# Performance work log

Measured on AMD Instinct MI355X. Metric: run time of the kernel, lower is better.

Reference implementation:

```python
import jax, jax.numpy as jnp
import numpy as np

DIM = 384
WIN = 7
HEADS = 12
HEAD_DIM = DIM // HEADS
N = WIN * WIN


def _relative_position_index(w):
    coords = np.stack(np.meshgrid(np.arange(w), np.arange(w), indexing='ij'))  # [2,w,w]
    cf = coords.reshape(2, -1)                                                 # [2,N]
    rel = cf[:, :, None] - cf[:, None, :]                                      # [2,N,N]
    rel = rel.transpose(1, 2, 0).copy()
    rel[:, :, 0] += w - 1
    rel[:, :, 1] += w - 1
    rel[:, :, 0] *= 2 * w - 1
    return jnp.asarray(rel.sum(-1), dtype=jnp.int32)                           # [N,N]


def setup_inputs() -> dict:
    key = jax.random.key(0)
    ks = jax.random.split(key, 6)
    B_ = 2048
    x = jax.random.normal(ks[0], (B_, N, DIM), dtype=jnp.float32)
    mask = jnp.zeros((64, N, N), dtype=bool)  # nW=64, all-unmasked but exercises mask path
    qkv_w = jax.random.normal(ks[1], (3 * DIM, DIM), dtype=jnp.float32) * 0.02
    qkv_b = jnp.zeros((3 * DIM,), dtype=jnp.float32)
    proj_w = jax.random.normal(ks[2], (DIM, DIM), dtype=jnp.float32) * 0.02
    proj_b = jnp.zeros((DIM,), dtype=jnp.float32)
    rpb_table = jax.random.normal(ks[3], ((2 * WIN - 1) ** 2, HEADS), dtype=jnp.float32) * 0.02
    rel_index = _relative_position_index(WIN)
    return {"x": x, "mask": mask, "qkv_w": qkv_w, "qkv_b": qkv_b,
            "proj_w": proj_w, "proj_b": proj_b, "rpb_table": rpb_table,
            "rel_index": rel_index}


def reference(x, mask, qkv_w, qkv_b, proj_w, proj_b, rpb_table, rel_index):
    B_, n, C = x.shape
    scale = HEAD_DIM ** -0.5
    # qkv projection -> [3, B, H, N, hd]
    qkv = (x @ qkv_w.T + qkv_b).reshape(B_, n, 3, HEADS, HEAD_DIM)
    qkv = jnp.transpose(qkv, (2, 0, 3, 1, 4))
    q, k, v = qkv[0], qkv[1], qkv[2]
    attn = jnp.einsum('bhnd,bhmd->bhnm', q, k) * scale  # [B,H,N,N]
    # relative position bias: gather [N*N,H] -> [H,N,N]
    bias = rpb_table[rel_index.reshape(-1)].reshape(n, n, HEADS)
    attn = attn + jnp.transpose(bias, (2, 0, 1))[None]
    nW = mask.shape[0]
    attn = attn.reshape(B_ // nW, nW, HEADS, n, n)
    attn = jnp.where(mask[None, :, None], -jnp.inf, attn)
    attn = attn.reshape(B_, HEADS, n, n)
    attn = jax.nn.softmax(attn, axis=-1)
    out = jnp.einsum('bhnm,bhmd->bnhd', attn, v).reshape(B_, n, C)
    return out @ proj_w.T + proj_b
```

## Files before the change

kernel.cpp:

```cpp
#include <hip/hip_runtime.h>
#include <stdint.h>

#define HEADS 12
#define HD 32
#define NTOK 49
#define DIM 384
#define SCALE 0.17677669529663687f

typedef __attribute__((ext_vector_type(8))) short s8v;
typedef __attribute__((ext_vector_type(4))) float f4v;

__device__ __forceinline__ unsigned short f2bf(float f) {
    union { float f; unsigned int i; } c; c.f = f;
    unsigned int x = c.i;
    return (unsigned short)((x + 0x7FFFu + ((x >> 16) & 1u)) >> 16);
}

__device__ __forceinline__ s8v load_pack8(const float* p) {
    float4 a = *(const float4*)p;
    float4 b = *(const float4*)(p + 4);
    s8v r;
    r[0] = (short)f2bf(a.x); r[1] = (short)f2bf(a.y);
    r[2] = (short)f2bf(a.z); r[3] = (short)f2bf(a.w);
    r[4] = (short)f2bf(b.x); r[5] = (short)f2bf(b.y);
    r[6] = (short)f2bf(b.z); r[7] = (short)f2bf(b.w);
    return r;
}

#define QFRAGS (12 * 12 * 6 * 64)
#define PFRAGS (12 * 24 * 64)
__device__ s8v qpack_g[QFRAGS];
__device__ s8v ppack_g[PFRAGS];

__global__ __launch_bounds__(256) void prepack(
    const float* __restrict__ qkvw, const float* __restrict__ projw)
{
    int t = blockIdx.x * 256 + threadIdx.x;
    if (t < QFRAGS) {
        int lane = t & 63, fid = t >> 6;
        int nt = fid % 6, ks = (fid / 6) % 12, h = fid / 72;
        int l15 = lane & 15, lq = lane >> 4;
        int c96 = nt * 16 + l15;
        int sect = c96 >> 5, cc = c96 & 31;
        const float* src = qkvw + (size_t)(sect * DIM + h * HD + cc) * DIM + ks * 32 + lq * 8;
        float s = (sect == 0) ? SCALE : 1.0f;
        float4 a = *(const float4*)src;
        float4 b = *(const float4*)(src + 4);
        s8v r;
        r[0] = (short)f2bf(a.x * s); r[1] = (short)f2bf(a.y * s);
        r[2] = (short)f2bf(a.z * s); r[3] = (short)f2bf(a.w * s);
        r[4] = (short)f2bf(b.x * s); r[5] = (short)f2bf(b.y * s);
        r[6] = (short)f2bf(b.z * s); r[7] = (short)f2bf(b.w * s);
        qpack_g[t] = r;
    } else if (t < QFRAGS + PFRAGS) {
        int u = t - QFRAGS;
        int lane = u & 63, fid = u >> 6;
        int ct = fid % 24, h = fid / 24;
        int l15 = lane & 15, lq = lane >> 4;
        const float* src = projw + (size_t)(ct * 16 + l15) * DIM + h * HD + lq * 8;
        ppack_g[u] = load_pack8(src);
    }
}

#define QK_OFF 0
#define VT_OFF 5120
#define PL_OFF 7424
#define HO_OFF 12032
#define LDS_TOT 14592

__global__ __launch_bounds__(256, 2) void winattn_fused(
    const float* __restrict__ xg,
    const unsigned char* __restrict__ maskg,
    const float* __restrict__ qkvb,
    const float* __restrict__ projb,
    const float* __restrict__ rpb,
    const int*   __restrict__ relidx,
    float*       __restrict__ outg)
{
    __shared__ __align__(16) unsigned short lds[LDS_TOT];
    const int tid = threadIdx.x;
    const int w   = tid >> 6;
    const int l   = tid & 63;
    const int l15 = l & 15;
    const int lq  = l >> 4;
    const int b   = blockIdx.x;

    const float*         xw    = xg + (size_t)b * (NTOK * DIM);
    const unsigned char* maskw = maskg + (size_t)(b & 63) * (NTOK * NTOK);

    const int arow = min(w * 16 + l15, NTOK - 1);
    s8v xa[12];
#pragma unroll
    for (int ks = 0; ks < 12; ++ks)
        xa[ks] = load_pack8(xw + arow * DIM + ks * 32 + lq * 8);

    int boff[4][4];
#pragma unroll
    for (int nt = 0; nt < 4; ++nt)
#pragma unroll
        for (int reg = 0; reg < 4; ++reg) {
            int i = w * 16 + lq * 4 + reg;
            int j = nt * 16 + l15;
            if (i < NTOK && j < NTOK)
                boff[nt][reg] = maskw[i * NTOK + j] ? -1 : relidx[i * NTOK + j] * (HEADS * 4);
            else
                boff[nt][reg] = (j >= NTOK) ? -1 : 0;
        }

    const f4v fz = {0.f, 0.f, 0.f, 0.f};
    f4v oc[4][6];
#pragma unroll
    for (int mt = 0; mt < 4; ++mt)
#pragma unroll
        for (int j = 0; j < 6; ++j) oc[mt][j] = fz;

    for (int h = 0; h < HEADS; ++h) {
        const s8v* qp = qpack_g + (size_t)h * (12 * 6 * 64) + l;
        f4v acc[6];
#pragma unroll
        for (int nt = 0; nt < 6; ++nt) acc[nt] = fz;
#pragma unroll
        for (int ks = 0; ks < 12; ++ks) {
            s8v a = xa[ks];
            s8v b0 = qp[(ks * 6 + 0) * 64];
            s8v b1 = qp[(ks * 6 + 1) * 64];
            s8v b2 = qp[(ks * 6 + 2) * 64];
            s8v b3 = qp[(ks * 6 + 3) * 64];
            s8v b4 = qp[(ks * 6 + 4) * 64];
            s8v b5 = qp[(ks * 6 + 5) * 64];
            acc[0] = __builtin_amdgcn_mfma_f32_16x16x32_bf16(a, b0, acc[0], 0, 0, 0);
            acc[1] = __builtin_amdgcn_mfma_f32_16x16x32_bf16(a, b1, acc[1], 0, 0, 0);
            acc[2] = __builtin_amdgcn_mfma_f32_16x16x32_bf16(a, b2, acc[2], 0, 0, 0);
            acc[3] = __builtin_amdgcn_mfma_f32_16x16x32_bf16(a, b3, acc[3], 0, 0, 0);
            acc[4] = __builtin_amdgcn_mfma_f32_16x16x32_bf16(a, b4, acc[4], 0, 0, 0);
            acc[5] = __builtin_amdgcn_mfma_f32_16x16x32_bf16(a, b5, acc[5], 0, 0, 0);
        }

        __syncthreads();

#pragma unroll
        for (int nt = 0; nt < 6; ++nt) {
            int c96 = nt * 16 + l15;
            int sect = c96 >> 5;
            int cc = c96 & 31;
            float bias = qkvb[sect * DIM + h * HD + cc];
            if (sect == 0) bias *= SCALE;
#pragma unroll
            for (int reg = 0; reg < 4; ++reg) {
                int row = w * 16 + lq * 4 + reg;
                float v = acc[nt][reg] + bias;
                unsigned short bv = f2bf(v);
                if (sect < 2) lds[QK_OFF + sect * 2560 + row * 40 + cc] = bv;
                else          lds[VT_OFF + cc * 72 + row] = bv;
            }
        }
        __syncthreads();

        s8v qa = *(const s8v*)(&lds[QK_OFF + (w * 16 + l15) * 40 + lq * 8]);
        f4v sc[4];
#pragma unroll
        for (int nt = 0; nt < 4; ++nt) {
            s8v kb = *(const s8v*)(&lds[QK_OFF + 2560 + (nt * 16 + l15) * 40 + lq * 8]);
            sc[nt] = __builtin_amdgcn_mfma_f32_16x16x32_bf16(qa, kb, fz, 0, 0, 0);
        }
        const char* rpbb = (const char*)rpb + h * 4;
#pragma unroll
        for (int nt = 0; nt < 4; ++nt)
#pragma unroll
            for (int reg = 0; reg < 4; ++reg) {
                int bo = boff[nt][reg];
                float v = sc[nt][reg] + *(const float*)(rpbb + (bo < 0 ? 0 : bo));
                sc[nt][reg] = (bo < 0) ? -1e30f : v;
            }
#pragma unroll
        for (int reg = 0; reg < 4; ++reg) {
            float m = fmaxf(fmaxf(sc[0][reg], sc[1][reg]), fmaxf(sc[2][reg], sc[3][reg]));
            m = fmaxf(m, __shfl_xor(m, 1));
            m = fmaxf(m, __shfl_xor(m, 2));
            m = fmaxf(m, __shfl_xor(m, 4));
            m = fmaxf(m, __shfl_xor(m, 8));
            float e0 = __expf(sc[0][reg] - m);
            float e1 = __expf(sc[1][reg] - m);
            float e2 = __expf(sc[2][reg] - m);
            float e3 = __expf(sc[3][reg] - m);
            float t = (e0 + e1) + (e2 + e3);
            t += __shfl_xor(t, 1);
            t += __shfl_xor(t, 2);
            t += __shfl_xor(t, 4);
            t += __shfl_xor(t, 8);
            float inv = 1.0f / t;
            sc[0][reg] = e0 * inv; sc[1][reg] = e1 * inv;
            sc[2][reg] = e2 * inv; sc[3][reg] = e3 * inv;
        }
#pragma unroll
        for (int nt = 0; nt < 4; ++nt)
#pragma unroll
            for (int reg = 0; reg < 4; ++reg) {
                int row = w * 16 + lq * 4 + reg;
                lds[PL_OFF + row * 72 + nt * 16 + l15] = f2bf(sc[nt][reg]);
            }

        f4v ho[2] = {fz, fz};
#pragma unroll
        for (int ks = 0; ks < 2; ++ks) {
            s8v pa = *(const s8v*)(&lds[PL_OFF + (w * 16 + l15) * 72 + ks * 32 + lq * 8]);
#pragma unroll
            for (int nt = 0; nt < 2; ++nt) {
                s8v vb = *(const s8v*)(&lds[VT_OFF + (nt * 16 + l15) * 72 + ks * 32 + lq * 8]);
                ho[nt] = __builtin_amdgcn_mfma_f32_16x16x32_bf16(pa, vb, ho[nt], 0, 0, 0);
            }
        }
#pragma unroll
        for (int nt = 0; nt < 2; ++nt)
#pragma unroll
            for (int reg = 0; reg < 4; ++reg) {
                int row = w * 16 + lq * 4 + reg;
                lds[HO_OFF + row * 40 + nt * 16 + l15] = f2bf(ho[nt][reg]);
            }
        __syncthreads();

        s8v ha[4];
#pragma unroll
        for (int mt = 0; mt < 4; ++mt)
            ha[mt] = *(const s8v*)(&lds[HO_OFF + (mt * 16 + l15) * 40 + lq * 8]);
        const s8v* pp = ppack_g + (size_t)h * (24 * 64) + l;
#pragma unroll
        for (int j = 0; j < 6; ++j) {
            s8v pb = pp[(w * 6 + j) * 64];
#pragma unroll
            for (int mt = 0; mt < 4; ++mt)
                oc[mt][j] = __builtin_amdgcn_mfma_f32_16x16x32_bf16(ha[mt], pb, oc[mt][j], 0, 0, 0);
        }
    }

#pragma unroll
    for (int j = 0; j < 6; ++j) {
        int col = (w * 6 + j) * 16 + l15;
        float pbv = projb[col];
#pragma unroll
        for (int mt = 0; mt < 4; ++mt)
#pragma unroll
            for (int reg = 0; reg < 4; ++reg) {
                int row = mt * 16 + lq * 4 + reg;
                if (row < NTOK)
                    outg[(size_t)b * (NTOK * DIM) + row * DIM + col] =
                        oc[mt][j][reg] + pbv;
            }
    }
}

extern "C" void kernel_launch(void* const* d_in, const int* in_sizes, int n_in,
                              void* d_out, int out_size, void* d_ws, size_t ws_size,
                              hipStream_t stream) {
    (void)n_in; (void)d_ws; (void)ws_size; (void)out_size;
    const int B = in_sizes[0] / (NTOK * DIM);
    hipLaunchKernelGGL(prepack, dim3((QFRAGS + PFRAGS) / 256), dim3(256), 0, stream,
        (const float*)d_in[2],
        (const float*)d_in[4]);
    hipLaunchKernelGGL(winattn_fused, dim3(B), dim3(256), 0, stream,
        (const float*)        d_in[0],
        (const unsigned char*)d_in[1],
        (const float*)        d_in[3],
        (const float*)        d_in[5],
        (const float*)        d_in[6],
        (const int*)          d_in[7],
        (float*)              d_out);
}
```

Baseline: 1.268 ms.

## Stage QKV weight fragments through double-buffered LDS with async global_load_lds

```diff
diff --git a/kernel.cpp b/kernel.cpp
--- a/kernel.cpp
+++ b/kernel.cpp
@@ -65,8 +65,29 @@
 #define QK_OFF 0
 #define VT_OFF 5120
 #define PL_OFF 7424
-#define HO_OFF 12032
-#define LDS_TOT 14592
+#define WB_OFF 12032
+#define LDS_TOT (12032 + 2 * 9216)
+
+__device__ __forceinline__ void stage18(const char* g, char* lbase, int w, int l) {
+    for (int i = w; i < 18; i += 4)
+        __builtin_amdgcn_global_load_lds(
+            (const __attribute__((address_space(1))) void*)(g + i * 1024 + l * 16),
+            (__attribute__((address_space(3))) void*)(lbase + i * 1024),
+            16, 0, 0);
+}
+
+__device__ __forceinline__ void chunkA(const unsigned short* fb0, const s8v* xa,
+                                       int k0, f4v* acc) {
+#pragma unroll
+    for (int ksl = 0; ksl < 3; ++ksl) {
+        s8v a = xa[k0 + ksl];
+        const unsigned short* fb = fb0 + ksl * 3072;
+#pragma unroll
+        for (int nt = 0; nt < 6; ++nt)
+            acc[nt] = __builtin_amdgcn_mfma_f32_16x16x32_bf16(
+                a, *(const s8v*)(fb + nt * 512), acc[nt], 0, 0, 0);
+    }
+}
 
 __global__ __launch_bounds__(256, 2) void winattn_fused(
     const float* __restrict__ xg,
@@ -87,6 +108,7 @@
 
     const float*         xw    = xg + (size_t)b * (NTOK * DIM);
     const unsigned char* maskw = maskg + (size_t)(b & 63) * (NTOK * NTOK);
+    char* const wb0 = (char*)lds + (WB_OFF * 2);
 
     const int arow = min(w * 16 + l15, NTOK - 1);
     s8v xa[12];
@@ -114,29 +136,30 @@
 #pragma unroll
         for (int j = 0; j < 6; ++j) oc[mt][j] = fz;
 
+    stage18((const char*)qpack_g, wb0, w, l);
+
     for (int h = 0; h < HEADS; ++h) {
-        const s8v* qp = qpack_g + (size_t)h * (12 * 6 * 64) + l;
+        const char* wsrc = (const char*)qpack_g + (size_t)h * 73728;
+        const unsigned short* fbl = &lds[WB_OFF] + l * 8;
+
+        __syncthreads();
+
         f4v acc[6];
 #pragma unroll
         for (int nt = 0; nt < 6; ++nt) acc[nt] = fz;
-#pragma unroll
-        for (int ks = 0; ks < 12; ++ks) {
-            s8v a = xa[ks];
-            s8v b0 = qp[(ks * 6 + 0) * 64];
-            s8v b1 = qp[(ks * 6 + 1) * 64];
-            s8v b2 = qp[(ks * 6 + 2) * 64];
-            s8v b3 = qp[(ks * 6 + 3) * 64];
-            s8v b4 = qp[(ks * 6 + 4) * 64];
-            s8v b5 = qp[(ks * 6 + 5) * 64];
-            acc[0] = __builtin_amdgcn_mfma_f32_16x16x32_bf16(a, b0, acc[0], 0, 0, 0);
-            acc[1] = __builtin_amdgcn_mfma_f32_16x16x32_bf16(a, b1, acc[1], 0, 0, 0);
-            acc[2] = __builtin_amdgcn_mfma_f32_16x16x32_bf16(a, b2, acc[2], 0, 0, 0);
-            acc[3] = __builtin_amdgcn_mfma_f32_16x16x32_bf16(a, b3, acc[3], 0, 0, 0);
-            acc[4] = __builtin_amdgcn_mfma_f32_16x16x32_bf16(a, b4, acc[4], 0, 0, 0);
-            acc[5] = __builtin_amdgcn_mfma_f32_16x16x32_bf16(a, b5, acc[5], 0, 0, 0);
-        }
-
-        __syncthreads();
+
+        stage18(wsrc + 18432, wb0 + 18432, w, l);
+        chunkA(fbl, xa, 0, acc);
+        __syncthreads();
+        stage18(wsrc + 2 * 18432, wb0, w, l);
+        chunkA(fbl + 9216, xa, 3, acc);
+        __syncthreads();
+        stage18(wsrc + 3 * 18432, wb0 + 18432, w, l);
+        chunkA(fbl, xa, 6, acc);
+        __syncthreads();
+        if (h < HEADS - 1)
+            stage18(wsrc + 73728, wb0, w, l);
+        chunkA(fbl + 9216, xa, 9, acc);
 
 #pragma unroll
         for (int nt = 0; nt < 6; ++nt) {
@@ -156,6 +179,21 @@
         }
         __syncthreads();
 
+        s8v pb[6];
+        const s8v* pp = ppack_g + (size_t)h * (24 * 64) + l;
+#pragma unroll
+        for (int j = 0; j < 6; ++j) pb[j] = pp[(w * 6 + j) * 64];
+
+        float bvv[4][4];
+        const char* rpbb = (const char*)rpb + h * 4;
+#pragma unroll
+        for (int nt = 0; nt < 4; ++nt)
+#pragma unroll
+            for (int reg = 0; reg < 4; ++reg) {
+                int bo = boff[nt][reg];
+                bvv[nt][reg] = *(const float*)(rpbb + (bo < 0 ? 0 : bo));
+            }
+
         s8v qa = *(const s8v*)(&lds[QK_OFF + (w * 16 + l15) * 40 + lq * 8]);
         f4v sc[4];
 #pragma unroll
@@ -163,14 +201,12 @@
             s8v kb = *(const s8v*)(&lds[QK_OFF + 2560 + (nt * 16 + l15) * 40 + lq * 8]);
             sc[nt] = __builtin_amdgcn_mfma_f32_16x16x32_bf16(qa, kb, fz, 0, 0, 0);
         }
-        const char* rpbb = (const char*)rpb + h * 4;
 #pragma unroll
         for (int nt = 0; nt < 4; ++nt)
 #pragma unroll
             for (int reg = 0; reg < 4; ++reg) {
-                int bo = boff[nt][reg];
-                float v = sc[nt][reg] + *(const float*)(rpbb + (bo < 0 ? 0 : bo));
-                sc[nt][reg] = (bo < 0) ? -1e30f : v;
+                float v = sc[nt][reg] + bvv[nt][reg];
+                sc[nt][reg] = (boff[nt][reg] < 0) ? -1e30f : v;
             }
 #pragma unroll
         for (int reg = 0; reg < 4; ++reg) {
@@ -215,21 +251,19 @@
 #pragma unroll
             for (int reg = 0; reg < 4; ++reg) {
                 int row = w * 16 + lq * 4 + reg;
-                lds[HO_OFF + row * 40 + nt * 16 + l15] = f2bf(ho[nt][reg]);
+                lds[PL_OFF + row * 72 + nt * 16 + l15] = f2bf(ho[nt][reg]);
             }
         __syncthreads();
 
         s8v ha[4];
 #pragma unroll
         for (int mt = 0; mt < 4; ++mt)
-            ha[mt] = *(const s8v*)(&lds[HO_OFF + (mt * 16 + l15) * 40 + lq * 8]);
-        const s8v* pp = ppack_g + (size_t)h * (24 * 64) + l;
+            ha[mt] = *(const s8v*)(&lds[PL_OFF + (mt * 16 + l15) * 72 + lq * 8]);
 #pragma unroll
         for (int j = 0; j < 6; ++j) {
-            s8v pb = pp[(w * 6 + j) * 64];
 #pragma unroll
             for (int mt = 0; mt < 4; ++mt)
-                oc[mt][j] = __builtin_amdgcn_mfma_f32_16x16x32_bf16(ha[mt], pb, oc[mt][j], 0, 0, 0);
+                oc[mt][j] = __builtin_amdgcn_mfma_f32_16x16x32_bf16(ha[mt], pb[j], oc[mt][j], 0, 0, 0);
         }
     }
 
```

New measurement: 1.085 ms. 1.17x faster.
